# Performance work log

Hardware: AMD Instinct MI355X
Metric: run time of the kernel (lower is better)

## Reference

```python
import jax, jax.numpy as jnp
import numpy as np

EXTENT = 0.5       # init kwarg 'extent'
RES = 256          # init kwarg 'resolution'
BATCH = 8
N_PTS = 65536      # one 256x256 Fourier slice per image


def setup_inputs() -> dict:
    key = jax.random.key(0)
    k1, k2 = jax.random.split(key)
    # coordinates in [-extent, extent]
    x = (jax.random.uniform(k1, (BATCH, N_PTS, 3), dtype=jnp.float32) * 2.0 - 1.0) * EXTENT
    # learned volume parameter, matches 1e-5 * randn init
    volume = 1e-5 * jax.random.normal(k2, (RES, RES, RES), dtype=jnp.float32)
    return {"x": x, "volume": volume}


def _grid_sample_3d(vol, coords):
    """Trilinear grid sample, align_corners=False, padding_mode='zeros'.
    vol: [D, H, W]; coords: [..., 3] with (x, y, z) in [-1, 1] indexing (W, H, D).
    Matches torch.nn.functional.grid_sample(mode='bilinear') for 5D input.
    """
    D, H, W = vol.shape
    gx, gy, gz = coords[..., 0], coords[..., 1], coords[..., 2]
    # unnormalize (align_corners=False): ix = ((x + 1) * W - 1) / 2
    ix = ((gx + 1.0) * W - 1.0) * 0.5
    iy = ((gy + 1.0) * H - 1.0) * 0.5
    iz = ((gz + 1.0) * D - 1.0) * 0.5
    x0 = jnp.floor(ix)
    y0 = jnp.floor(iy)
    z0 = jnp.floor(iz)
    tx = ix - x0  # fractional weights
    ty = iy - y0
    tz = iz - z0
    x0i = x0.astype(jnp.int32)
    y0i = y0.astype(jnp.int32)
    z0i = z0.astype(jnp.int32)

    def corner(dz, dy, dx):
        xi = x0i + dx
        yi = y0i + dy
        zi = z0i + dz
        valid = (xi >= 0) & (xi < W) & (yi >= 0) & (yi < H) & (zi >= 0) & (zi < D)
        v = vol[jnp.clip(zi, 0, D - 1), jnp.clip(yi, 0, H - 1), jnp.clip(xi, 0, W - 1)]
        return jnp.where(valid, v, jnp.zeros((), vol.dtype))

    wx0, wy0, wz0 = 1.0 - tx, 1.0 - ty, 1.0 - tz
    out = (corner(0, 0, 0) * wz0 * wy0 * wx0
           + corner(0, 0, 1) * wz0 * wy0 * tx
           + corner(0, 1, 0) * wz0 * ty * wx0
           + corner(0, 1, 1) * wz0 * ty * tx
           + corner(1, 0, 0) * tz * wy0 * wx0
           + corner(1, 0, 1) * tz * wy0 * tx
           + corner(1, 1, 0) * tz * ty * wx0
           + corner(1, 1, 1) * tz * ty * tx)
    return out


def reference(x, volume):
    # original: grid_sample(100 * volume.repeat(B,...), x/(2*extent)*2)
    #    the linear interpolation (mathematically identical).
    coords = x / EXTENT  # [B, n_pts, 3] in [-1, 1]
    return 100.0 * _grid_sample_3d(volume, coords)  # [B, n_pts]
```

## Files before the change

kernel.cpp:

```cpp
#include <hip/hip_runtime.h>


#define RES 256

__device__ __forceinline__ void point_setup(
    const float* __restrict__ x, int i,
    int& r00, int& r01, int& r10, int& r11, int& xc0, int& xc1,
    float& wx0, float& wx1, float& wy0, float& wy1, float& wz0, float& wz1)
{
    float gx = __builtin_nontemporal_load(&x[3 * i + 0]) * 2.0f;
    float gy = __builtin_nontemporal_load(&x[3 * i + 1]) * 2.0f;
    float gz = __builtin_nontemporal_load(&x[3 * i + 2]) * 2.0f;

    float ix = ((gx + 1.0f) * (float)RES - 1.0f) * 0.5f;
    float iy = ((gy + 1.0f) * (float)RES - 1.0f) * 0.5f;
    float iz = ((gz + 1.0f) * (float)RES - 1.0f) * 0.5f;

    float x0f = floorf(ix), y0f = floorf(iy), z0f = floorf(iz);
    float tx = ix - x0f, ty = iy - y0f, tz = iz - z0f;

    int x0 = (int)x0f, y0 = (int)y0f, z0 = (int)z0f;
    int x1 = x0 + 1, y1 = y0 + 1, z1 = z0 + 1;

    wx0 = (x0 >= 0 && x0 < RES) ? (1.0f - tx) : 0.0f;
    wx1 = (x1 >= 0 && x1 < RES) ? tx : 0.0f;
    wy0 = (y0 >= 0 && y0 < RES) ? (1.0f - ty) : 0.0f;
    wy1 = (y1 >= 0 && y1 < RES) ? ty : 0.0f;
    wz0 = (z0 >= 0 && z0 < RES) ? (1.0f - tz) : 0.0f;
    wz1 = (z1 >= 0 && z1 < RES) ? tz : 0.0f;

    xc0 = min(max(x0, 0), RES - 1); xc1 = min(max(x1, 0), RES - 1);
    int yc0 = min(max(y0, 0), RES - 1), yc1 = min(max(y1, 0), RES - 1);
    int zc0 = min(max(z0, 0), RES - 1), zc1 = min(max(z1, 0), RES - 1);

    r00 = (zc0 * RES + yc0) * RES;
    r01 = (zc0 * RES + yc1) * RES;
    r10 = (zc1 * RES + yc0) * RES;
    r11 = (zc1 * RES + yc1) * RES;
}

__device__ __forceinline__ float trilerp(
    const float* __restrict__ vol,
    int r00, int r01, int r10, int r11, int xc0, int xc1,
    float wx0, float wx1, float wy0, float wy1, float wz0, float wz1)
{
    float v000 = vol[r00 + xc0];
    float v001 = vol[r00 + xc1];
    float v010 = vol[r01 + xc0];
    float v011 = vol[r01 + xc1];
    float v100 = vol[r10 + xc0];
    float v101 = vol[r10 + xc1];
    float v110 = vol[r11 + xc0];
    float v111 = vol[r11 + xc1];

    float c00 = v000 * wx0 + v001 * wx1;
    float c01 = v010 * wx0 + v011 * wx1;
    float c10 = v100 * wx0 + v101 * wx1;
    float c11 = v110 * wx0 + v111 * wx1;
    float c0 = c00 * wy0 + c01 * wy1;
    float c1 = c10 * wy0 + c11 * wy1;
    return 100.0f * (c0 * wz0 + c1 * wz1);
}

__global__ __launch_bounds__(256) void VolumeExplicit_29257317220866_kernel(
    const float* __restrict__ x,
    const float* __restrict__ vol,
    float* __restrict__ out,
    int n)
{
    int tid = blockIdx.x * blockDim.x + threadIdx.x;
    int half = n >> 1;
    if (tid >= half) return;
    int iA = tid;
    int iB = tid + half;

    int a_r00, a_r01, a_r10, a_r11, a_x0, a_x1;
    float a_wx0, a_wx1, a_wy0, a_wy1, a_wz0, a_wz1;
    point_setup(x, iA, a_r00, a_r01, a_r10, a_r11, a_x0, a_x1,
                a_wx0, a_wx1, a_wy0, a_wy1, a_wz0, a_wz1);

    int b_r00, b_r01, b_r10, b_r11, b_x0, b_x1;
    float b_wx0, b_wx1, b_wy0, b_wy1, b_wz0, b_wz1;
    point_setup(x, iB, b_r00, b_r01, b_r10, b_r11, b_x0, b_x1,
                b_wx0, b_wx1, b_wy0, b_wy1, b_wz0, b_wz1);

    float oA = trilerp(vol, a_r00, a_r01, a_r10, a_r11, a_x0, a_x1,
                       a_wx0, a_wx1, a_wy0, a_wy1, a_wz0, a_wz1);
    float oB = trilerp(vol, b_r00, b_r01, b_r10, b_r11, b_x0, b_x1,
                       b_wx0, b_wx1, b_wy0, b_wy1, b_wz0, b_wz1);

    __builtin_nontemporal_store(oA, &out[iA]);
    __builtin_nontemporal_store(oB, &out[iB]);
}

extern "C" void kernel_launch(void* const* d_in, const int* in_sizes, int n_in,
                              void* d_out, int out_size, void* d_ws, size_t ws_size,
                              hipStream_t stream) {
    const float* x   = (const float*)d_in[0];
    const float* vol = (const float*)d_in[1];
    float* out = (float*)d_out;

    int n = out_size;
    int half = n >> 1;
    int block = 256;
    int grid = (half + block - 1) / block;
    VolumeExplicit_29257317220866_kernel<<<grid, block, 0, stream>>>(x, vol, out, n);
}
```

Before: 120.9 us.

## Bin points by z-slice and gather per bucket with XCD-aware block mapping

Adds a two-pass path. The scatter kernel buckets points by their rounded z index into 256 buckets of fixed capacity, using shared-memory histograms and global atomic cursors. A gather kernel then interpolates each bucket, mapping buckets to blocks so that z-adjacent buckets land on the same XCD. The goal is L2 locality for volume reads, which are random in the original. In exchange it adds a memset, an extra kernel launch, and a write and read of the sorted buffer. Points that overflow a bucket are interpolated directly in the scatter kernel, and the path only runs for n == 524288 with enough workspace.

Measured after the change: 138.0 us. +14.2%, slower.

```diff
diff --git a/kernel.cpp b/kernel.cpp
--- a/kernel.cpp
+++ b/kernel.cpp
@@ -2,15 +2,22 @@
 
 
 #define RES 256
-
-__device__ __forceinline__ void point_setup(
-    const float* __restrict__ x, int i,
+#define NB 256
+#define CAP 2560
+#define SLOTS_PER_SUB 512
+#define SUBS 5
+
+typedef float vfloat4 __attribute__((ext_vector_type(4)));
+
+
+__device__ __forceinline__ void setup_c(
+    float rx, float ry, float rz,
     int& r00, int& r01, int& r10, int& r11, int& xc0, int& xc1,
     float& wx0, float& wx1, float& wy0, float& wy1, float& wz0, float& wz1)
 {
-    float gx = __builtin_nontemporal_load(&x[3 * i + 0]) * 2.0f;
-    float gy = __builtin_nontemporal_load(&x[3 * i + 1]) * 2.0f;
-    float gz = __builtin_nontemporal_load(&x[3 * i + 2]) * 2.0f;
+    float gx = rx * 2.0f;
+    float gy = ry * 2.0f;
+    float gz = rz * 2.0f;
 
     float ix = ((gx + 1.0f) * (float)RES - 1.0f) * 0.5f;
     float iy = ((gy + 1.0f) * (float)RES - 1.0f) * 0.5f;
@@ -37,6 +44,18 @@
     r01 = (zc0 * RES + yc1) * RES;
     r10 = (zc1 * RES + yc0) * RES;
     r11 = (zc1 * RES + yc1) * RES;
+}
+
+__device__ __forceinline__ void point_setup(
+    const float* __restrict__ x, int i,
+    int& r00, int& r01, int& r10, int& r11, int& xc0, int& xc1,
+    float& wx0, float& wx1, float& wy0, float& wy1, float& wz0, float& wz1)
+{
+    float rx = __builtin_nontemporal_load(&x[3 * i + 0]);
+    float ry = __builtin_nontemporal_load(&x[3 * i + 1]);
+    float rz = __builtin_nontemporal_load(&x[3 * i + 2]);
+    setup_c(rx, ry, rz, r00, r01, r10, r11, xc0, xc1,
+            wx0, wx1, wy0, wy1, wz0, wz1);
 }
 
 __device__ __forceinline__ float trilerp(
@@ -62,6 +81,121 @@
     return 100.0f * (c0 * wz0 + c1 * wz1);
 }
 
+__device__ __forceinline__ float interp_point(
+    const float* __restrict__ vol, float rx, float ry, float rz)
+{
+    int r00, r01, r10, r11, x0, x1;
+    float wx0, wx1, wy0, wy1, wz0, wz1;
+    setup_c(rx, ry, rz, r00, r01, r10, r11, x0, x1,
+            wx0, wx1, wy0, wy1, wz0, wz1);
+    return trilerp(vol, r00, r01, r10, r11, x0, x1,
+                   wx0, wx1, wy0, wy1, wz0, wz1);
+}
+
+
+__global__ __launch_bounds__(256) void VolumeExplicit_scatter_kernel(
+    const float* __restrict__ x,
+    const float* __restrict__ vol,
+    float* __restrict__ out,
+    vfloat4* __restrict__ sorted,
+    unsigned* __restrict__ cursor)
+{
+    __shared__ unsigned lh[NB];
+    __shared__ unsigned lbase[NB];
+    int t = threadIdx.x;
+    int base_i = blockIdx.x * 1024;
+
+    lh[t] = 0;
+    __syncthreads();
+
+    float px[4], py[4], pz[4];
+    int bk[4];
+    unsigned lr[4];
+    #pragma unroll
+    for (int k = 0; k < 4; ++k) {
+        int i = base_i + (k << 8) + t;
+        px[k] = __builtin_nontemporal_load(&x[3 * i + 0]);
+        py[k] = __builtin_nontemporal_load(&x[3 * i + 1]);
+        pz[k] = __builtin_nontemporal_load(&x[3 * i + 2]);
+        float iz = ((pz[k] * 2.0f + 1.0f) * (float)RES - 1.0f) * 0.5f;
+        int b = (int)(iz + 0.5f);
+        b = min(max(b, 0), NB - 1);
+        bk[k] = b;
+        lr[k] = atomicAdd(&lh[b], 1u);
+    }
+    __syncthreads();
+
+    unsigned c = lh[t];
+    lbase[t] = c ? atomicAdd(&cursor[t], c) : 0u;
+    __syncthreads();
+
+    #pragma unroll
+    for (int k = 0; k < 4; ++k) {
+        int i = base_i + (k << 8) + t;
+        unsigned pos = lbase[bk[k]] + lr[k];
+        if (pos < CAP) {
+            vfloat4 v;
+            v.x = px[k]; v.y = py[k]; v.z = pz[k];
+            v.w = __uint_as_float((unsigned)i);
+            sorted[bk[k] * CAP + pos] = v;
+        } else {
+            out[i] = interp_point(vol, px[k], py[k], pz[k]);
+        }
+    }
+}
+
+
+__global__ __launch_bounds__(256) void VolumeExplicit_gather_kernel(
+    const vfloat4* __restrict__ sorted,
+    const unsigned* __restrict__ cursor,
+    const float* __restrict__ vol,
+    float* __restrict__ out)
+{
+    int t = threadIdx.x;
+    int B = blockIdx.x;
+    int xcd = B & 7;
+    int r = B >> 3;
+    int j = r & 15;
+    int sub = r >> 4;
+
+    #pragma unroll 1
+    for (int h = 0; h < 2; ++h) {
+        int bucket = xcd * 32 + h * 16 + j;
+        unsigned count = min(cursor[bucket], (unsigned)CAP);
+        if (count == 0) continue;
+        int cm1 = (int)count - 1;
+
+        int sA = sub * SLOTS_PER_SUB + t;
+        int sB = sA + 256;
+        bool vA = sA < (int)count;
+        bool vB = sB < (int)count;
+        int sAc = min(sA, cm1);
+        int sBc = min(sB, cm1);
+
+        vfloat4 pA = __builtin_nontemporal_load(&sorted[bucket * CAP + sAc]);
+        vfloat4 pB = __builtin_nontemporal_load(&sorted[bucket * CAP + sBc]);
+
+        int a_r00, a_r01, a_r10, a_r11, a_x0, a_x1;
+        float a_wx0, a_wx1, a_wy0, a_wy1, a_wz0, a_wz1;
+        setup_c(pA.x, pA.y, pA.z, a_r00, a_r01, a_r10, a_r11, a_x0, a_x1,
+                a_wx0, a_wx1, a_wy0, a_wy1, a_wz0, a_wz1);
+
+        int b_r00, b_r01, b_r10, b_r11, b_x0, b_x1;
+        float b_wx0, b_wx1, b_wy0, b_wy1, b_wz0, b_wz1;
+        setup_c(pB.x, pB.y, pB.z, b_r00, b_r01, b_r10, b_r11, b_x0, b_x1,
+                b_wx0, b_wx1, b_wy0, b_wy1, b_wz0, b_wz1);
+
+        float oA = trilerp(vol, a_r00, a_r01, a_r10, a_r11, a_x0, a_x1,
+                           a_wx0, a_wx1, a_wy0, a_wy1, a_wz0, a_wz1);
+        float oB = trilerp(vol, b_r00, b_r01, b_r10, b_r11, b_x0, b_x1,
+                           b_wx0, b_wx1, b_wy0, b_wy1, b_wz0, b_wz1);
+
+        if (vA) out[__float_as_uint(pA.w)] = oA;
+        if (vB) out[__float_as_uint(pB.w)] = oB;
+    }
+}
+
+
 __global__ __launch_bounds__(256) void VolumeExplicit_29257317220866_kernel(
     const float* __restrict__ x,
     const float* __restrict__ vol,
@@ -101,8 +235,21 @@
     float* out = (float*)d_out;
 
     int n = out_size;
-    int half = n >> 1;
-    int block = 256;
-    int grid = (half + block - 1) / block;
-    VolumeExplicit_29257317220866_kernel<<<grid, block, 0, stream>>>(x, vol, out, n);
-}
+    size_t need = 4096 + (size_t)NB * CAP * sizeof(vfloat4);
+
+    if (n == 524288 && d_ws != nullptr && ws_size >= need) {
+        unsigned* cursor = (unsigned*)d_ws;
+        vfloat4* sorted  = (vfloat4*)((char*)d_ws + 4096);
+
+        hipMemsetAsync(cursor, 0, NB * sizeof(unsigned), stream);
+        VolumeExplicit_scatter_kernel<<<n / 1024, 256, 0, stream>>>(
+            x, vol, out, sorted, cursor);
+        VolumeExplicit_gather_kernel<<<8 * 16 * SUBS, 256, 0, stream>>>(
+            sorted, cursor, vol, out);
+    } else {
+        int half = n >> 1;
+        int block = 256;
+        int grid = (half + block - 1) / block;
+        VolumeExplicit_29257317220866_kernel<<<grid, block, 0, stream>>>(x, vol, out, n);
+    }
+}
```
